# Kernel tuning notes

Measured on AMD Instinct MI355X. Metric: run time of the kernel, lower is better.

Reference implementation:

```python
import jax, jax.numpy as jnp
import numpy as np

NEG_SLOPE = 0.01  # torch nn.LeakyReLU default


def setup_inputs() -> dict:
    key = jax.random.key(0)
    ks = jax.random.split(key, 6)
    B, L, C, D = 4, 1024, 128, 64
    return {
        "queries": jax.random.normal(ks[0], (B, L, C), dtype=jnp.float32),
        "keys": jax.random.normal(ks[1], (B, L, C), dtype=jnp.float32),
        "values": jax.random.normal(ks[2], (B, L, C), dtype=jnp.float32),
        "linear_l": jax.random.normal(ks[3], (C, D), dtype=jnp.float32) * 0.05,
        "linear_r": jax.random.normal(ks[4], (C, D), dtype=jnp.float32) * 0.05,
        "a": jax.random.normal(ks[5], (D, 1), dtype=jnp.float32) * 0.05,
    }


def reference(queries, keys, values, linear_l, linear_r, a):
    # keys/values are accepted by the torch forward but unused in its math.
    # g_l, g_r: (B, L, D)
    g_l = jnp.einsum('blc,cd->bld', queries, linear_l)
    g_r = jnp.einsum('blc,cd->bld', queries, linear_r)
    # torch repeat/repeat_interleave + view(b,l,l,-1) yields
    # g_sum[b, x, y] = g_l[b, y] + g_r[b, x]  -> (B, L, L, D)
    g_sum = g_l[:, None, :, :] + g_r[:, :, None, :]
    g_sum = jnp.where(g_sum >= 0, g_sum, NEG_SLOPE * g_sum)  # LeakyReLU
    e = jnp.einsum('bxyd,d->bxy', g_sum, a[:, 0])            # (B, L, L)
    scores = jax.nn.softmax(e, axis=-1)                       # dropout is identity in eval
    y = jnp.einsum('bxy,byd->bxd', scores, g_r)               # (B, L, D)
    return (y, scores)
```

## Files before the change

kernel.cpp:

```cpp
#include <hip/hip_runtime.h>
#include <math.h>

#define LL   1024
#define NROW 4096
#define DD   64
#define CC   128

#define C1H 0.505f
#define C2H 0.495f

typedef short  bf16x8 __attribute__((ext_vector_type(8)));
typedef float  f32x4  __attribute__((ext_vector_type(4)));

static __device__ __forceinline__ unsigned short bf16rne(float f) {
  unsigned u = __float_as_uint(f);
  u += 0x7fffu + ((u >> 16) & 1u);
  return (unsigned short)(u >> 16);
}

static __device__ __forceinline__ void unpk(unsigned u, float& lo, float& hi) {
  lo = __uint_as_float(u << 16);
  hi = __uint_as_float(u & 0xffff0000u);
}

static __device__ __forceinline__ float rflf(float v) {
  return __uint_as_float(__builtin_amdgcn_readfirstlane(__float_as_uint(v)));
}

__global__ __launch_bounds__(256) void k_proj(
    const float* __restrict__ q, const float* __restrict__ Wl,
    const float* __restrict__ Wr, const float* __restrict__ a,
    uint4* __restrict__ glg, float* __restrict__ gr,
    unsigned short* __restrict__ grT_bf,
    float* __restrict__ AL, float* __restrict__ AR) {
  const int bl0 = blockIdx.x * 8;
  const int b = bl0 >> 10;
  const int t = threadIdx.x;
  __shared__ __align__(16) float qs[8 * CC];
  __shared__ __align__(16) unsigned short trT[DD][8];
  __shared__ __align__(16) unsigned short trL[8][DD];

  ((float4*)qs)[t] = ((const float4*)(q + (size_t)bl0 * CC))[t];
  __syncthreads();

  const int rr = t >> 6;
  const int d  = t & 63;
  const int r0 = rr * 2, r1 = rr * 2 + 1;
  const float* q0 = qs + r0 * CC;
  const float* q1 = qs + r1 * CC;

  float aL0 = 0, aL1 = 0, aR0 = 0, aR1 = 0;
  float bL0 = 0, bL1 = 0, bR0 = 0, bR1 = 0;
#pragma unroll 8
  for (int c = 0; c < CC; c += 2) {
    float wl0 = Wl[c * DD + d],       wr0 = Wr[c * DD + d];
    float wl1 = Wl[(c + 1) * DD + d], wr1 = Wr[(c + 1) * DD + d];
    aL0 = fmaf(q0[c], wl0, aL0);  bL0 = fmaf(q0[c + 1], wl1, bL0);
    aL1 = fmaf(q1[c], wl0, aL1);  bL1 = fmaf(q1[c + 1], wl1, bL1);
    aR0 = fmaf(q0[c], wr0, aR0);  bR0 = fmaf(q0[c + 1], wr1, bR0);
    aR1 = fmaf(q1[c], wr0, aR1);  bR1 = fmaf(q1[c + 1], wr1, bR1);
  }
  float gL0 = aL0 + bL0, gL1 = aL1 + bL1;
  float gR0 = aR0 + bR0, gR1 = aR1 + bR1;

  trL[r0][d] = bf16rne(gL0);
  trL[r1][d] = bf16rne(gL1);
  gr[(size_t)(bl0 + r0) * DD + d] = gR0;
  gr[(size_t)(bl0 + r1) * DD + d] = gR1;
  trT[d][r0] = bf16rne(gR0);
  trT[d][r1] = bf16rne(gR1);

  float av = a[d];
  float vL0 = av * gL0, vL1 = av * gL1, vR0 = av * gR0, vR1 = av * gR1;
#pragma unroll
  for (int off = 1; off < 64; off <<= 1) {
    vL0 += __shfl_xor(vL0, off, 64);
    vL1 += __shfl_xor(vL1, off, 64);
    vR0 += __shfl_xor(vR0, off, 64);
    vR1 += __shfl_xor(vR1, off, 64);
  }
  if (d == 0) {
    AL[bl0 + r0] = vL0; AL[bl0 + r1] = vL1;
    AR[bl0 + r0] = vR0; AR[bl0 + r1] = vR1;
  }
  __syncthreads();
  if (t < 64) {
    *(uint4*)&grT_bf[(((size_t)(b * 64 + t)) << 10) + (bl0 & 1023)] =
        *(const uint4*)&trT[t][0];
  } else if (t < 128) {
    int tt = t - 64;
    int r = tt >> 3, g = tt & 7;
    glg[(((size_t)(b * 8 + g)) << 10) + (bl0 & 1023) + r] =
        *(const uint4*)&trL[r][g * 8];
  }
}

__global__ __launch_bounds__(256, 4) void k_fused(
    const uint4* __restrict__ glg, const float* __restrict__ gr,
    const unsigned short* __restrict__ grT_bf,
    const float* __restrict__ AL, const float* __restrict__ AR,
    const float* __restrict__ a,
    float* __restrict__ scores, float* __restrict__ yout) {
  const int bl0 = blockIdx.x * 4;
  const int b = bl0 >> 10;
  const int t = threadIdx.x;
  const int w = t >> 6, l = t & 63;

  __shared__ __align__(16) unsigned char pfrag[9216];
  __shared__ float sRedM[4][4], sRedS[4][4];
  __shared__ __align__(16) float sPV[4][4][16][4];

  float pr[4];
#pragma unroll
  for (int x = 0; x < 4; ++x) pr[x] = C1H * rflf(AR[bl0 + x]);

  float alv[4];
#pragma unroll
  for (int yc = 0; yc < 4; ++yc) alv[yc] = AL[b * LL + yc * 256 + t];

  float pacc[4][4];
#pragma unroll
  for (int x = 0; x < 4; ++x)
#pragma unroll
    for (int yc = 0; yc < 4; ++yc) pacc[x][yc] = 0.f;

#pragma unroll
  for (int dblk = 0; dblk < 4; ++dblk) {
    uint4 gv[4][2];
#pragma unroll
    for (int yc = 0; yc < 4; ++yc)
#pragma unroll
      for (int g2 = 0; g2 < 2; ++g2)
        gv[yc][g2] = glg[(((size_t)(b * 8 + dblk * 2 + g2)) << 10) + yc * 256 + t];

    float sa[16];
#pragma unroll
    for (int c4 = 0; c4 < 4; ++c4) {
      float4 v = *(const float4*)&a[dblk * 16 + c4 * 4];
      sa[c4 * 4 + 0] = rflf(v.x); sa[c4 * 4 + 1] = rflf(v.y);
      sa[c4 * 4 + 2] = rflf(v.z); sa[c4 * 4 + 3] = rflf(v.w);
    }
    float sgr[4][16];
#pragma unroll
    for (int x = 0; x < 4; ++x)
#pragma unroll
      for (int c4 = 0; c4 < 4; ++c4) {
        float4 v = *(const float4*)&gr[(size_t)(bl0 + x) * DD + dblk * 16 + c4 * 4];
        sgr[x][c4 * 4 + 0] = rflf(v.x); sgr[x][c4 * 4 + 1] = rflf(v.y);
        sgr[x][c4 * 4 + 2] = rflf(v.z); sgr[x][c4 * 4 + 3] = rflf(v.w);
      }

#pragma unroll
    for (int yc = 0; yc < 4; ++yc) {
      float glv[16];
      unpk(gv[yc][0].x, glv[0], glv[1]);   unpk(gv[yc][0].y, glv[2], glv[3]);
      unpk(gv[yc][0].z, glv[4], glv[5]);   unpk(gv[yc][0].w, glv[6], glv[7]);
      unpk(gv[yc][1].x, glv[8], glv[9]);   unpk(gv[yc][1].y, glv[10], glv[11]);
      unpk(gv[yc][1].z, glv[12], glv[13]); unpk(gv[yc][1].w, glv[14], glv[15]);
#pragma unroll
      for (int x = 0; x < 4; ++x) {
        float s = pacc[x][yc];
#pragma unroll
        for (int c = 0; c < 16; ++c)
          s = fmaf(fabsf(glv[c] + sgr[x][c]), sa[c], s);
        pacc[x][yc] = s;
      }
    }
  }

  float ev[4][4];
#pragma unroll
  for (int x = 0; x < 4; ++x)
#pragma unroll
    for (int yc = 0; yc < 4; ++yc)
      ev[x][yc] = fmaf(C2H, pacc[x][yc], pr[x] + C1H * alv[yc]);

  float lm[4];
#pragma unroll
  for (int x = 0; x < 4; ++x)
    lm[x] = fmaxf(fmaxf(ev[x][0], ev[x][1]), fmaxf(ev[x][2], ev[x][3]));
#pragma unroll
  for (int off = 1; off < 64; off <<= 1) {
#pragma unroll
    for (int x = 0; x < 4; ++x) lm[x] = fmaxf(lm[x], __shfl_xor(lm[x], off, 64));
  }
  if (l == 0) {
#pragma unroll
    for (int x = 0; x < 4; ++x) sRedM[w][x] = lm[x];
  }
  __syncthreads();

  float mfin[4], lsum[4];
#pragma unroll
  for (int x = 0; x < 4; ++x)
    mfin[x] = fmaxf(fmaxf(sRedM[0][x], sRedM[1][x]),
                    fmaxf(sRedM[2][x], sRedM[3][x]));
#pragma unroll
  for (int x = 0; x < 4; ++x) {
    lsum[x] = 0.f;
#pragma unroll
    for (int yc = 0; yc < 4; ++yc) {
      ev[x][yc] = __expf(ev[x][yc] - mfin[x]);
      lsum[x] += ev[x][yc];
    }
  }
#pragma unroll
  for (int off = 1; off < 64; off <<= 1) {
#pragma unroll
    for (int x = 0; x < 4; ++x) lsum[x] += __shfl_xor(lsum[x], off, 64);
  }
  if (l == 0) {
#pragma unroll
    for (int x = 0; x < 4; ++x) sRedS[w][x] = lsum[x];
  }
  __syncthreads();

  float isv[4];
#pragma unroll
  for (int x = 0; x < 4; ++x)
    isv[x] = 1.0f / (sRedS[0][x] + sRedS[1][x] + sRedS[2][x] + sRedS[3][x]);

  unsigned short* eb = (unsigned short*)pfrag;
  const int hq = (t >> 3) & 3, jq = t & 7, kq = t >> 5;
#pragma unroll
  for (int yc = 0; yc < 4; ++yc) {
    int y = yc * 256 + t;
    int kc = yc * 8 + kq;
#pragma unroll
    for (int x = 0; x < 4; ++x) {
      float p = ev[x][yc] * isv[x];
      __builtin_nontemporal_store(p, &scores[((size_t)(bl0 + x) << 10) + y]);
      eb[kc * 128 + (4 * x + hq) * 8 + jq] = bf16rne(p);
    }
  }
  __syncthreads();

  f32x4 acc[4] = {{0.f, 0.f, 0.f, 0.f}, {0.f, 0.f, 0.f, 0.f},
                  {0.f, 0.f, 0.f, 0.f}, {0.f, 0.f, 0.f, 0.f}};
  const int row16 = l & 15, hh = l >> 4;
  const size_t bnBase = ((size_t)b * 64) << 10;
#pragma unroll
  for (int kk = 0; kk < 8; ++kk) {
    int kc = w + kk * 4;
    bf16x8 af = *(const bf16x8*)(pfrag + kc * 256 + (4 * row16 + hh) * 16);
#pragma unroll
    for (int nt = 0; nt < 4; ++nt) {
      bf16x8 bfv = *(const bf16x8*)(grT_bf + bnBase +
                     (((size_t)(nt * 16 + row16)) << 10) + kc * 32 + hh * 8);
      acc[nt] = __builtin_amdgcn_mfma_f32_16x16x32_bf16(af, bfv, acc[nt], 0, 0, 0);
    }
  }
  if (l < 16) {
#pragma unroll
    for (int nt = 0; nt < 4; ++nt)
#pragma unroll
      for (int i = 0; i < 4; ++i) sPV[w][nt][l][i] = acc[nt][i];
  }
  __syncthreads();
  if (t < 64) {
    int nt = t >> 4, col = t & 15;
#pragma unroll
    for (int i = 0; i < 4; ++i) {
      float r = sPV[0][nt][col][i] + sPV[1][nt][col][i] +
                sPV[2][nt][col][i] + sPV[3][nt][col][i];
      yout[(size_t)(bl0 + i) * DD + nt * 16 + col] = r;
    }
  }
}

extern "C" void kernel_launch(void* const* d_in, const int* in_sizes, int n_in,
                              void* d_out, int out_size, void* d_ws, size_t ws_size,
                              hipStream_t stream) {
  const float* q  = (const float*)d_in[0];
  const float* Wl = (const float*)d_in[3];
  const float* Wr = (const float*)d_in[4];
  const float* a  = (const float*)d_in[5];

  float* yout = (float*)d_out;
  float* esc  = yout + NROW * DD;

  float* ws = (float*)d_ws;
  float* gr = ws;
  float* AL = gr + NROW * DD;
  float* AR = AL + NROW;
  uint4* glg = (uint4*)(AR + NROW);
  unsigned short* grT_bf = (unsigned short*)(glg + (size_t)NROW * 8);

  k_proj <<<NROW / 8, 256, 0, stream>>>(q, Wl, Wr, a, glg, gr, grT_bf, AL, AR);
  k_fused<<<NROW / 4, 256, 0, stream>>>(glg, gr, grT_bf, AL, AR, a, esc, yout);
}
```

Before: 40.75 us.

## Split fused softmax and PV into separate scores and PV kernels

Splits the fused kernel into k_e, which computes and stores the softmax scores with normal instead of nontemporal stores, and a new k_pv kernel that reads the scores back, converts them to bf16 and runs the PV MFMA with 16 rows per block. The old per-block 4-row MFMA reuse was wasteful (16-row tiles with 4 valid rows), so the new layout is meant to use MFMA rows fully and shrink LDS in the scores kernel. The cost is an extra launch and a 16 MB re-read of the scores from global memory or cache.

```diff
diff --git a/kernel.cpp b/kernel.cpp
--- a/kernel.cpp
+++ b/kernel.cpp
@@ -95,20 +95,17 @@
   }
 }
 
-__global__ __launch_bounds__(256, 4) void k_fused(
+__global__ __launch_bounds__(256, 4) void k_e(
     const uint4* __restrict__ glg, const float* __restrict__ gr,
-    const unsigned short* __restrict__ grT_bf,
     const float* __restrict__ AL, const float* __restrict__ AR,
     const float* __restrict__ a,
-    float* __restrict__ scores, float* __restrict__ yout) {
+    float* __restrict__ scores) {
   const int bl0 = blockIdx.x * 4;
   const int b = bl0 >> 10;
   const int t = threadIdx.x;
   const int w = t >> 6, l = t & 63;
 
-  __shared__ __align__(16) unsigned char pfrag[9216];
   __shared__ float sRedM[4][4], sRedS[4][4];
-  __shared__ __align__(16) float sPV[4][4][16][4];
 
   float pr[4];
 #pragma unroll
@@ -220,51 +217,64 @@
   for (int x = 0; x < 4; ++x)
     isv[x] = 1.0f / (sRedS[0][x] + sRedS[1][x] + sRedS[2][x] + sRedS[3][x]);
 
-  unsigned short* eb = (unsigned short*)pfrag;
-  const int hq = (t >> 3) & 3, jq = t & 7, kq = t >> 5;
 #pragma unroll
   for (int yc = 0; yc < 4; ++yc) {
     int y = yc * 256 + t;
-    int kc = yc * 8 + kq;
-#pragma unroll
-    for (int x = 0; x < 4; ++x) {
-      float p = ev[x][yc] * isv[x];
-      __builtin_nontemporal_store(p, &scores[((size_t)(bl0 + x) << 10) + y]);
-      eb[kc * 128 + (4 * x + hq) * 8 + jq] = bf16rne(p);
-    }
-  }
-  __syncthreads();
+#pragma unroll
+    for (int x = 0; x < 4; ++x)
+      scores[((size_t)(bl0 + x) << 10) + y] = ev[x][yc] * isv[x];
+  }
+}
+
+__global__ __launch_bounds__(512) void k_pv(
+    const float* __restrict__ scores, const unsigned short* __restrict__ grT_bf,
+    float* __restrict__ yout) {
+  const int bl0 = blockIdx.x * 16;
+  const int b = bl0 >> 10;
+  const int t = threadIdx.x;
+  const int w = t >> 6, l = t & 63;
+  const int row16 = l & 15, hh = l >> 4;
+
+  __shared__ float sPV[8][4][16][17];
 
   f32x4 acc[4] = {{0.f, 0.f, 0.f, 0.f}, {0.f, 0.f, 0.f, 0.f},
                   {0.f, 0.f, 0.f, 0.f}, {0.f, 0.f, 0.f, 0.f}};
-  const int row16 = l & 15, hh = l >> 4;
   const size_t bnBase = ((size_t)b * 64) << 10;
-#pragma unroll
-  for (int kk = 0; kk < 8; ++kk) {
-    int kc = w + kk * 4;
-    bf16x8 af = *(const bf16x8*)(pfrag + kc * 256 + (4 * row16 + hh) * 16);
+  const float* arow = scores + ((size_t)(bl0 + row16) << 10);
+
+#pragma unroll
+  for (int kk = 0; kk < 4; ++kk) {
+    const int kc = w + kk * 8;
+    float4 f0 = *(const float4*)&arow[kc * 32 + hh * 8];
+    float4 f1 = *(const float4*)&arow[kc * 32 + hh * 8 + 4];
+    union { unsigned short us[8]; bf16x8 v; } af;
+    af.us[0] = bf16rne(f0.x); af.us[1] = bf16rne(f0.y);
+    af.us[2] = bf16rne(f0.z); af.us[3] = bf16rne(f0.w);
+    af.us[4] = bf16rne(f1.x); af.us[5] = bf16rne(f1.y);
+    af.us[6] = bf16rne(f1.z); af.us[7] = bf16rne(f1.w);
 #pragma unroll
     for (int nt = 0; nt < 4; ++nt) {
       bf16x8 bfv = *(const bf16x8*)(grT_bf + bnBase +
                      (((size_t)(nt * 16 + row16)) << 10) + kc * 32 + hh * 8);
-      acc[nt] = __builtin_amdgcn_mfma_f32_16x16x32_bf16(af, bfv, acc[nt], 0, 0, 0);
+      acc[nt] = __builtin_amdgcn_mfma_f32_16x16x32_bf16(af.v, bfv, acc[nt], 0, 0, 0);
     }
   }
-  if (l < 16) {
-#pragma unroll
-    for (int nt = 0; nt < 4; ++nt)
-#pragma unroll
-      for (int i = 0; i < 4; ++i) sPV[w][nt][l][i] = acc[nt][i];
-  }
-  __syncthreads();
-  if (t < 64) {
-    int nt = t >> 4, col = t & 15;
-#pragma unroll
-    for (int i = 0; i < 4; ++i) {
-      float r = sPV[0][nt][col][i] + sPV[1][nt][col][i] +
-                sPV[2][nt][col][i] + sPV[3][nt][col][i];
-      yout[(size_t)(bl0 + i) * DD + nt * 16 + col] = r;
-    }
+
+#pragma unroll
+  for (int nt = 0; nt < 4; ++nt)
+#pragma unroll
+    for (int i = 0; i < 4; ++i)
+      sPV[w][nt][hh * 4 + i][row16] = acc[nt][i];
+  __syncthreads();
+
+#pragma unroll
+  for (int rep = 0; rep < 2; ++rep) {
+    int o = t + rep * 512;
+    int x = o >> 6, dcol = o & 63, nt = dcol >> 4, col = dcol & 15;
+    float r = 0.f;
+#pragma unroll
+    for (int ww = 0; ww < 8; ++ww) r += sPV[ww][nt][x][col];
+    yout[(size_t)(bl0 + x) * DD + dcol] = r;
   }
 }
 
@@ -286,6 +296,7 @@
   uint4* glg = (uint4*)(AR + NROW);
   unsigned short* grT_bf = (unsigned short*)(glg + (size_t)NROW * 8);
 
-  k_proj <<<NROW / 8, 256, 0, stream>>>(q, Wl, Wr, a, glg, gr, grT_bf, AL, AR);
-  k_fused<<<NROW / 4, 256, 0, stream>>>(glg, gr, grT_bf, AL, AR, a, esc, yout);
-}
+  k_proj<<<NROW / 8, 256, 0, stream>>>(q, Wl, Wr, a, glg, gr, grT_bf, AL, AR);
+  k_e   <<<NROW / 4, 256, 0, stream>>>(glg, gr, AL, AR, a, esc);
+  k_pv  <<<NROW / 16, 512, 0, stream>>>(esc, grT_bf, yout);
+}
```

After: 47.01 us. 15.3% more time.
